# Performance work log

Hardware: AMD Instinct MI355X
Metric: run time of the kernel (lower is better)

The kernel has to match this reference:

```python
import jax, jax.numpy as jnp
import numpy as np

HEADS = 8
DIM_HEAD = 32
SCALE = DIM_HEAD ** -0.5


def setup_inputs() -> dict:
    key = jax.random.key(0)
    k1, k2, k3 = jax.random.split(key, 3)
    B, H, W, C = 16, 64, 64, 256
    hidden = HEADS * DIM_HEAD  # 256
    x = jax.random.normal(k1, (B, H, W, C), dtype=jnp.float32)
    # 1x1 convs with no bias == dense matmuls over channel dim (glorot-ish scale)
    w_qkv = jax.random.normal(k2, (C, 3 * hidden), dtype=jnp.float32) * (1.0 / np.sqrt(C))
    w_out = jax.random.normal(k3, (hidden, C), dtype=jnp.float32) * (1.0 / np.sqrt(hidden))
    return {"x": x, "w_qkv": w_qkv, "w_out": w_out}


def reference(x, w_qkv, w_out):
    B, H, W, C = x.shape
    n = H * W
    # to_qkv: 1x1 conv, no bias
    qkv = jnp.einsum('bhwc,cf->bhwf', x, w_qkv)  # [B,H,W,3*hidden]
    q, k, v = jnp.split(qkv, 3, axis=-1)

    def to_heads(t):
        # 'b x y (h c) -> b h c (x y)'
        t = t.reshape(B, n, HEADS, DIM_HEAD)
        return jnp.transpose(t, (0, 2, 3, 1))  # [B, heads, dim_head, n]

    q, k, v = to_heads(q), to_heads(k), to_heads(v)
    q = jax.nn.softmax(q, axis=-2) * SCALE      # softmax over feature dim d
    k = jax.nn.softmax(k, axis=-1)              # softmax over spatial dim n
    context = jnp.einsum('bhdn,bhen->bhde', k, v)   # [B, heads, d, e]
    out = jnp.einsum('bhde,bhdn->bhen', context, q)  # [B, heads, e, n]
    # 'b h c (x y) -> b x y (h c)'
    out = jnp.transpose(out, (0, 3, 1, 2)).reshape(B, H, W, HEADS * DIM_HEAD)
    # to_out: 1x1 conv, no bias
    return jnp.einsum('bhwf,fc->bhwc', out, w_out)
```

## Files before the change

kernel.cpp:

```cpp
#include <hip/hip_runtime.h>

using short8 = __attribute__((ext_vector_type(8))) short;
using f32x4  = __attribute__((ext_vector_type(4))) float;

#define SCALE_Q 0.17677669529663687f
#define NCHUNK 16

__device__ __forceinline__ unsigned short f2bf(float f) {
  unsigned u = __float_as_uint(f);
  return (unsigned short)((u + 0x7FFFu + ((u >> 16) & 1u)) >> 16);
}
__device__ __forceinline__ float bf2f(unsigned h) { return __uint_as_float(h << 16); }

__device__ __forceinline__ void bf8_to_f(uint4 r, float* o) {
  o[0] = bf2f(r.x & 0xffffu); o[1] = bf2f(r.x >> 16);
  o[2] = bf2f(r.y & 0xffffu); o[3] = bf2f(r.y >> 16);
  o[4] = bf2f(r.z & 0xffffu); o[5] = bf2f(r.z >> 16);
  o[6] = bf2f(r.w & 0xffffu); o[7] = bf2f(r.w >> 16);
}

__device__ __forceinline__ void gl_lds16(const unsigned short* g, unsigned short* l) {
  __builtin_amdgcn_global_load_lds(
      (const __attribute__((address_space(1))) void*)g,
      (__attribute__((address_space(3))) void*)l, 16, 0, 0);
}

__global__ __launch_bounds__(256) void prep_kernel(
    const float* __restrict__ x, const float* __restrict__ wqkv, const float* __restrict__ wout,
    unsigned short* __restrict__ xb, unsigned short* __restrict__ wqkvT,
    unsigned short* __restrict__ woutT) {
  const int blk = blockIdx.x;
  if (blk < 16384) {
    const size_t i = ((size_t)blk * 256 + threadIdx.x) * 4;
    const float4 v = *(const float4*)(x + i);
    *(ushort4*)(xb + i) = make_ushort4(f2bf(v.x), f2bf(v.y), f2bf(v.z), f2bf(v.w));
  } else if (blk < 16384 + 768) {
    const int n = blk - 16384, k = threadIdx.x;
    wqkvT[n * 256 + k] = f2bf(wqkv[(size_t)k * 768 + n]);
  } else {
    const int c = blk - 16384 - 768, f = threadIdx.x;
    woutT[c * 256 + f] = f2bf(wout[(size_t)f * 256 + c]);
  }
}

template <typename OutT, bool QSOFT, bool SWZ>
__global__ __launch_bounds__(256) void gemm_bt(
    const unsigned short* __restrict__ A, const unsigned short* __restrict__ BT,
    OutT* __restrict__ D, unsigned short* __restrict__ QS,
    int nbn, int K, int N,
    size_t strideA, size_t strideB, size_t strideD) {
  __shared__ unsigned short As[128 * 64];
  __shared__ unsigned short Bs[128 * 64];
  int lin = blockIdx.x;
  if (SWZ) {
    const int cpx = gridDim.x >> 3;
    lin = (lin & 7) * cpx + (lin >> 3);
  }
  const int bn = lin % nbn, bm = lin / nbn, bz = blockIdx.z;
  const int tid = threadIdx.x, lane = tid & 63, wid = tid >> 6;
  const int wr = wid >> 1, wc = wid & 1;
  const int fr = lane & 15, hi = lane >> 4;
  f32x4 acc[4][4] = {};
  const unsigned short* Ab = A + (size_t)bz * strideA + (size_t)bm * 128 * K;
  const unsigned short* Bb = BT + (size_t)bz * strideB + (size_t)bn * 128 * K;

  const int srow = wid * 32 + (lane >> 3);
  const int scol = (lane & 7) * 8;
  const unsigned short* Ap = Ab + (size_t)srow * K + scol;
  const unsigned short* Bp = Bb + (size_t)srow * K + scol;
  unsigned short* Asw = As + (wid * 4) * 512 + 0;
  unsigned short* Bsw = Bs + (wid * 4) * 512 + 0;

  for (int kt = 0; kt < K; kt += 64) {
#pragma unroll
    for (int i = 0; i < 4; ++i) {
      gl_lds16(Ap + (size_t)i * 8 * K + kt, Asw + i * 512);
      gl_lds16(Bp + (size_t)i * 8 * K + kt, Bsw + i * 512);
    }
    __syncthreads();
#pragma unroll
    for (int kk = 0; kk < 2; ++kk) {
      short8 af[4], bfv[4];
#pragma unroll
      for (int i = 0; i < 4; ++i) {
        af[i]  = *(const short8*)&As[(wr * 64 + i * 16 + fr) * 64 + kk * 32 + hi * 8];
        bfv[i] = *(const short8*)&Bs[(wc * 64 + i * 16 + fr) * 64 + kk * 32 + hi * 8];
      }
#pragma unroll
      for (int mi = 0; mi < 4; ++mi)
#pragma unroll
        for (int nj = 0; nj < 4; ++nj)
          acc[mi][nj] = __builtin_amdgcn_mfma_f32_16x16x32_bf16(af[mi], bfv[nj], acc[mi][nj], 0, 0, 0);
    }
    __syncthreads();
  }

  const size_t r0 = (size_t)bm * 128 + wr * 64;
  if (QSOFT && bn < 2) {
    const int c0 = bn * 128 + wc * 64;
#pragma unroll
    for (int mi = 0; mi < 4; ++mi)
#pragma unroll
      for (int p = 0; p < 2; ++p)
#pragma unroll
        for (int r = 0; r < 4; ++r) {
          const float v0 = acc[mi][2 * p][r], v1 = acc[mi][2 * p + 1][r];
          float mx = fmaxf(v0, v1);
#pragma unroll
          for (int xm = 1; xm < 16; xm <<= 1) mx = fmaxf(mx, __shfl_xor(mx, xm, 64));
          const float e0 = __expf(v0 - mx), e1 = __expf(v1 - mx);
          float s = e0 + e1;
#pragma unroll
          for (int xm = 1; xm < 16; xm <<= 1) s += __shfl_xor(s, xm, 64);
          const float inv = SCALE_Q / s;
          const size_t row = r0 + mi * 16 + hi * 4 + r;
          QS[row * 256 + c0 + p * 32 + fr]      = f2bf(e0 * inv);
          QS[row * 256 + c0 + p * 32 + 16 + fr] = f2bf(e1 * inv);
        }
    return;
  }
  const int colbase = (QSOFT ? (bn - 2) : bn) * 128 + wc * 64;
  OutT* Dz = D + (size_t)bz * strideD;
#pragma unroll
  for (int mi = 0; mi < 4; ++mi)
#pragma unroll
    for (int nj = 0; nj < 4; ++nj) {
      const int col = colbase + nj * 16 + fr;
#pragma unroll
      for (int r = 0; r < 4; ++r) {
        const size_t row = r0 + mi * 16 + hi * 4 + r;
        const float v = acc[mi][nj][r];
        if constexpr (sizeof(OutT) == 2) Dz[row * N + col] = (OutT)f2bf(v);
        else                             Dz[row * N + col] = v;
      }
    }
}

__global__ __launch_bounds__(256) void ctx_part_kernel(const unsigned short* __restrict__ kv,
                                                       float* __restrict__ part,
                                                       float* __restrict__ spart) {
  const int blk = blockIdx.x;
  const int bh = blk >> 4, chunk = blk & 15;
  const int b = bh >> 3, h = bh & 7;
  const int tid = threadIdx.x, d = tid & 31, g = tid >> 5;
  const unsigned short* kbase =
      kv + (size_t)b * 4096 * 512 + h * 32 + (size_t)chunk * 256 * 512;
  const unsigned short* vbase = kbase + 256;

  __shared__ float ek[64][36], vv[64][36];
  float a0 = 0.f, a1 = 0.f, a2 = 0.f, a3 = 0.f, ssum = 0.f;
  const int e0 = g * 4;
  const int sn = tid >> 2, sc = (tid & 3) * 8;
  const unsigned short* kp0 = kbase + (size_t)sn * 512 + sc;
  const unsigned short* vp0 = vbase + (size_t)sn * 512 + sc;
  uint4 kr = *(const uint4*)kp0;
  uint4 vr = *(const uint4*)vp0;
  for (int n0 = 0; n0 < 256; n0 += 64) {
    float kf[8], vf[8];
    bf8_to_f(kr, kf); bf8_to_f(vr, vf);
    uint4 krn = kr, vrn = vr;
    if (n0 + 64 < 256) {
      krn = *(const uint4*)(kp0 + (size_t)(n0 + 64) * 512);
      vrn = *(const uint4*)(vp0 + (size_t)(n0 + 64) * 512);
    }
#pragma unroll
    for (int j = 0; j < 8; ++j) { ek[sn][sc + j] = __expf(kf[j]); vv[sn][sc + j] = vf[j]; }
    __syncthreads();
#pragma unroll 8
    for (int i = 0; i < 64; ++i) {
      const float kd = ek[i][d];
      const float4 v4 = *(const float4*)&vv[i][e0];
      ssum += kd;
      a0 += kd * v4.x; a1 += kd * v4.y; a2 += kd * v4.z; a3 += kd * v4.w;
    }
    __syncthreads();
    kr = krn; vr = vrn;
  }
  float* pp = part + ((size_t)chunk * 128 + bh) * 1024 + d * 32 + e0;
  pp[0] = a0; pp[1] = a1; pp[2] = a2; pp[3] = a3;
  if (g == 0) spart[((size_t)chunk * 128 + bh) * 32 + d] = ssum;
}

__global__ __launch_bounds__(256) void ctx_combine_kernel(const float* __restrict__ part,
                                                          const float* __restrict__ spart,
                                                          float* __restrict__ ctx) {
  const int bh = blockIdx.x, tid = threadIdx.x;
  __shared__ float sinv[32];
  if (tid < 32) {
    float s = 0.f;
#pragma unroll
    for (int c = 0; c < NCHUNK; ++c) s += spart[((size_t)c * 128 + bh) * 32 + tid];
    sinv[tid] = 1.0f / s;
  }
  __syncthreads();
  float4 acc = make_float4(0.f, 0.f, 0.f, 0.f);
#pragma unroll
  for (int c = 0; c < NCHUNK; ++c) {
    const float4 p = *(const float4*)(part + ((size_t)c * 128 + bh) * 1024 + tid * 4);
    acc.x += p.x; acc.y += p.y; acc.z += p.z; acc.w += p.w;
  }
  const float si = sinv[tid >> 3];
  float4* cp = (float4*)(ctx + (size_t)bh * 1024 + tid * 4);
  *cp = make_float4(acc.x * si, acc.y * si, acc.z * si, acc.w * si);
}

__global__ __launch_bounds__(256) void w2_kernel(const float* __restrict__ ctx,
                                                 const unsigned short* __restrict__ woutT,
                                                 unsigned short* __restrict__ W2T) {
  const int b = blockIdx.x >> 4, cg = blockIdx.x & 15;
  const int tid = threadIdx.x;
  __shared__ float cs[8 * 32 * 32];
  {
    const float4* src = (const float4*)(ctx + (size_t)b * 8192);
    float4* dst = (float4*)cs;
#pragma unroll
    for (int i = 0; i < 8; ++i) dst[tid + i * 256] = src[tid + i * 256];
  }
  __syncthreads();
  const int c = cg * 16 + (tid >> 4), chunk = tid & 15;
  const int h = chunk >> 1, d0 = (chunk & 1) * 16;
  float wf[32];
  {
    const uint4* wp = (const uint4*)(woutT + (size_t)c * 256 + h * 32);
    bf8_to_f(wp[0], wf + 0); bf8_to_f(wp[1], wf + 8);
    bf8_to_f(wp[2], wf + 16); bf8_to_f(wp[3], wf + 24);
  }
  unsigned short o[16];
#pragma unroll
  for (int dd = 0; dd < 16; ++dd) {
    const float* cp = cs + h * 1024 + (d0 + dd) * 32;
    float acc = 0.f;
#pragma unroll
    for (int e = 0; e < 32; ++e) acc += cp[e] * wf[e];
    o[dd] = f2bf(acc);
  }
  uint4* op = (uint4*)(W2T + ((size_t)b * 256 + c) * 256 + chunk * 16);
  op[0] = make_uint4((unsigned)o[0] | ((unsigned)o[1] << 16), (unsigned)o[2] | ((unsigned)o[3] << 16),
                     (unsigned)o[4] | ((unsigned)o[5] << 16), (unsigned)o[6] | ((unsigned)o[7] << 16));
  op[1] = make_uint4((unsigned)o[8] | ((unsigned)o[9] << 16), (unsigned)o[10] | ((unsigned)o[11] << 16),
                     (unsigned)o[12] | ((unsigned)o[13] << 16), (unsigned)o[14] | ((unsigned)o[15] << 16));
}

extern "C" void kernel_launch(void* const* d_in, const int* in_sizes, int n_in,
                              void* d_out, int out_size, void* d_ws, size_t ws_size,
                              hipStream_t stream) {
  const float* x     = (const float*)d_in[0];
  const float* wqkv  = (const float*)d_in[1];
  const float* wout  = (const float*)d_in[2];
  float* out = (float*)d_out;

  char* ws = (char*)d_ws;
  unsigned short* xb    = (unsigned short*)(ws);
  unsigned short* wqkvT = (unsigned short*)(ws + 33554432);
  unsigned short* woutT = (unsigned short*)(ws + 33947648);
  unsigned short* kv    = (unsigned short*)(ws + 34078720);
  float*          ctx   = (float*)        (ws + 101187584);
  unsigned short* qs    = (unsigned short*)(ws + 101711872);
  float*          part  = (float*)(ws);
  float*          spart = (float*)(ws + 8388608);
  unsigned short* W2T   = (unsigned short*)(ws + 12582912);

  prep_kernel<<<16384 + 768 + 256, 256, 0, stream>>>(x, wqkv, wout, xb, wqkvT, woutT);
  gemm_bt<unsigned short, true, true><<<3072, 256, 0, stream>>>(
      xb, wqkvT, kv, qs, 6, 256, 512, 0, 0, 0);
  ctx_part_kernel<<<2048, 256, 0, stream>>>(kv, part, spart);
  ctx_combine_kernel<<<128, 256, 0, stream>>>(part, spart, ctx);
  w2_kernel<<<256, 256, 0, stream>>>(ctx, woutT, W2T);
  gemm_bt<float, false, false><<<dim3(64, 1, 16), 256, 0, stream>>>(
      qs, W2T, out, nullptr, 2, 256, 256, (size_t)4096 * 256, (size_t)256 * 256, (size_t)4096 * 256);
}
```

Before: 175.0 us.

## Keep GEMM B strip in registers and stream full-K A tiles through swizzled LDS

Both GEMMs are replaced by a kernel in which each block loads a 64-column strip of the weight matrix into registers once. It then loops over several 128-row A tiles, loading the full K=256 into LDS with an XOR swizzle to avoid bank conflicts. This cuts repeated B traffic and the per-k-tile syncs, and maps groups of tiles to XCDs for L2 locality. In exchange it uses many more registers (128 VGPRs for B), a 64 KB LDS tile and no load/compute overlap within a block, so occupancy may drop.

```diff
diff --git a/kernel.cpp b/kernel.cpp
--- a/kernel.cpp
+++ b/kernel.cpp
@@ -43,97 +43,97 @@
   }
 }
 
-template <typename OutT, bool QSOFT, bool SWZ>
-__global__ __launch_bounds__(256) void gemm_bt(
+template <typename OutT, bool QKV>
+__global__ __launch_bounds__(256, 2) void gemm_bregs(
     const unsigned short* __restrict__ A, const unsigned short* __restrict__ BT,
     OutT* __restrict__ D, unsigned short* __restrict__ QS,
-    int nbn, int K, int N,
+    int NSTRIP, int TPB,
     size_t strideA, size_t strideB, size_t strideD) {
-  __shared__ unsigned short As[128 * 64];
-  __shared__ unsigned short Bs[128 * 64];
-  int lin = blockIdx.x;
-  if (SWZ) {
-    const int cpx = gridDim.x >> 3;
-    lin = (lin & 7) * cpx + (lin >> 3);
-  }
-  const int bn = lin % nbn, bm = lin / nbn, bz = blockIdx.z;
+  __shared__ unsigned short As[128 * 256];
+  const int xcd = blockIdx.x & 7, idx = blockIdx.x >> 3;
+  const int strip = idx % NSTRIP;
+  const int mg = xcd + (idx / NSTRIP) * 8;
+  const int z = blockIdx.z;
   const int tid = threadIdx.x, lane = tid & 63, wid = tid >> 6;
-  const int wr = wid >> 1, wc = wid & 1;
   const int fr = lane & 15, hi = lane >> 4;
-  f32x4 acc[4][4] = {};
-  const unsigned short* Ab = A + (size_t)bz * strideA + (size_t)bm * 128 * K;
-  const unsigned short* Bb = BT + (size_t)bz * strideB + (size_t)bn * 128 * K;
-
-  const int srow = wid * 32 + (lane >> 3);
-  const int scol = (lane & 7) * 8;
-  const unsigned short* Ap = Ab + (size_t)srow * K + scol;
-  const unsigned short* Bp = Bb + (size_t)srow * K + scol;
-  unsigned short* Asw = As + (wid * 4) * 512 + 0;
-  unsigned short* Bsw = Bs + (wid * 4) * 512 + 0;
-
-  for (int kt = 0; kt < K; kt += 64) {
-#pragma unroll
-    for (int i = 0; i < 4; ++i) {
-      gl_lds16(Ap + (size_t)i * 8 * K + kt, Asw + i * 512);
-      gl_lds16(Bp + (size_t)i * 8 * K + kt, Bsw + i * 512);
-    }
-    __syncthreads();
-#pragma unroll
-    for (int kk = 0; kk < 2; ++kk) {
-      short8 af[4], bfv[4];
-#pragma unroll
-      for (int i = 0; i < 4; ++i) {
-        af[i]  = *(const short8*)&As[(wr * 64 + i * 16 + fr) * 64 + kk * 32 + hi * 8];
-        bfv[i] = *(const short8*)&Bs[(wc * 64 + i * 16 + fr) * 64 + kk * 32 + hi * 8];
+
+  const unsigned short* Bb = BT + (size_t)z * strideB + (size_t)strip * 64 * 256;
+  short8 breg[4][8];
+#pragma unroll
+  for (int nj = 0; nj < 4; ++nj)
+#pragma unroll
+    for (int kk = 0; kk < 8; ++kk)
+      breg[nj][kk] = *(const short8*)(Bb + (size_t)(nj * 16 + fr) * 256 + kk * 32 + hi * 8);
+
+  const int srow = tid >> 5;
+  const int schunk = (tid & 31) ^ srow;
+  const size_t sgoff = (size_t)srow * 256 + schunk * 8;
+  unsigned short* lds_w = As + wid * 512;
+
+  for (int t = 0; t < TPB; ++t) {
+    const size_t row0 = (size_t)(mg * TPB + t) * 128;
+    const unsigned short* Ag = A + (size_t)z * strideA + row0 * 256 + sgoff;
+#pragma unroll
+    for (int r = 0; r < 16; ++r) gl_lds16(Ag + r * 2048, lds_w + r * 2048);
+    __syncthreads();
+
+    f32x4 acc[2][4] = {};
+#pragma unroll
+    for (int kk = 0; kk < 8; ++kk) {
+      short8 af[2];
+#pragma unroll
+      for (int mi = 0; mi < 2; ++mi) {
+        const int row = wid * 32 + mi * 16 + fr;
+        const int ch = (kk * 4 + hi) ^ (fr & 7);
+        af[mi] = *(const short8*)&As[row * 256 + ch * 8];
       }
 #pragma unroll
-      for (int mi = 0; mi < 4; ++mi)
+      for (int mi = 0; mi < 2; ++mi)
 #pragma unroll
         for (int nj = 0; nj < 4; ++nj)
-          acc[mi][nj] = __builtin_amdgcn_mfma_f32_16x16x32_bf16(af[mi], bfv[nj], acc[mi][nj], 0, 0, 0);
-    }
-    __syncthreads();
-  }
-
-  const size_t r0 = (size_t)bm * 128 + wr * 64;
-  if (QSOFT && bn < 2) {
-    const int c0 = bn * 128 + wc * 64;
-#pragma unroll
-    for (int mi = 0; mi < 4; ++mi)
-#pragma unroll
-      for (int p = 0; p < 2; ++p)
-#pragma unroll
-        for (int r = 0; r < 4; ++r) {
-          const float v0 = acc[mi][2 * p][r], v1 = acc[mi][2 * p + 1][r];
-          float mx = fmaxf(v0, v1);
-#pragma unroll
-          for (int xm = 1; xm < 16; xm <<= 1) mx = fmaxf(mx, __shfl_xor(mx, xm, 64));
-          const float e0 = __expf(v0 - mx), e1 = __expf(v1 - mx);
-          float s = e0 + e1;
-#pragma unroll
-          for (int xm = 1; xm < 16; xm <<= 1) s += __shfl_xor(s, xm, 64);
-          const float inv = SCALE_Q / s;
-          const size_t row = r0 + mi * 16 + hi * 4 + r;
-          QS[row * 256 + c0 + p * 32 + fr]      = f2bf(e0 * inv);
-          QS[row * 256 + c0 + p * 32 + 16 + fr] = f2bf(e1 * inv);
+          acc[mi][nj] = __builtin_amdgcn_mfma_f32_16x16x32_bf16(af[mi], breg[nj][kk], acc[mi][nj], 0, 0, 0);
+    }
+
+    if (QKV && strip < 4) {
+#pragma unroll
+      for (int mi = 0; mi < 2; ++mi)
+#pragma unroll
+        for (int p = 0; p < 2; ++p)
+#pragma unroll
+          for (int r = 0; r < 4; ++r) {
+            const float v0 = acc[mi][2 * p][r], v1 = acc[mi][2 * p + 1][r];
+            float mx = fmaxf(v0, v1);
+#pragma unroll
+            for (int xm = 1; xm < 16; xm <<= 1) mx = fmaxf(mx, __shfl_xor(mx, xm, 64));
+            const float e0 = __expf(v0 - mx), e1 = __expf(v1 - mx);
+            float s = e0 + e1;
+#pragma unroll
+            for (int xm = 1; xm < 16; xm <<= 1) s += __shfl_xor(s, xm, 64);
+            const float inv = SCALE_Q / s;
+            const size_t row = row0 + wid * 32 + mi * 16 + hi * 4 + r;
+            QS[row * 256 + strip * 64 + p * 32 + fr]      = f2bf(e0 * inv);
+            QS[row * 256 + strip * 64 + p * 32 + 16 + fr] = f2bf(e1 * inv);
+          }
+    } else {
+      const int c0 = QKV ? (strip * 64 - 256) : (strip * 64);
+      const int ncols = QKV ? 512 : 256;
+      OutT* Dz = D + (size_t)z * strideD;
+#pragma unroll
+      for (int mi = 0; mi < 2; ++mi)
+#pragma unroll
+        for (int nj = 0; nj < 4; ++nj) {
+          const int col = c0 + nj * 16 + fr;
+#pragma unroll
+          for (int r = 0; r < 4; ++r) {
+            const size_t row = row0 + wid * 32 + mi * 16 + hi * 4 + r;
+            const float v = acc[mi][nj][r];
+            if constexpr (sizeof(OutT) == 2) Dz[row * ncols + col] = (OutT)f2bf(v);
+            else                             Dz[row * ncols + col] = v;
+          }
         }
-    return;
-  }
-  const int colbase = (QSOFT ? (bn - 2) : bn) * 128 + wc * 64;
-  OutT* Dz = D + (size_t)bz * strideD;
-#pragma unroll
-  for (int mi = 0; mi < 4; ++mi)
-#pragma unroll
-    for (int nj = 0; nj < 4; ++nj) {
-      const int col = colbase + nj * 16 + fr;
-#pragma unroll
-      for (int r = 0; r < 4; ++r) {
-        const size_t row = r0 + mi * 16 + hi * 4 + r;
-        const float v = acc[mi][nj][r];
-        if constexpr (sizeof(OutT) == 2) Dz[row * N + col] = (OutT)f2bf(v);
-        else                             Dz[row * N + col] = v;
-      }
-    }
+    }
+    __syncthreads();
+  }
 }
 
 __global__ __launch_bounds__(256) void ctx_part_kernel(const unsigned short* __restrict__ kv,
@@ -261,11 +261,12 @@
   unsigned short* W2T   = (unsigned short*)(ws + 12582912);
 
   prep_kernel<<<16384 + 768 + 256, 256, 0, stream>>>(x, wqkv, wout, xb, wqkvT, woutT);
-  gemm_bt<unsigned short, true, true><<<3072, 256, 0, stream>>>(
-      xb, wqkvT, kv, qs, 6, 256, 512, 0, 0, 0);
+  gemm_bregs<unsigned short, true><<<1536, 256, 0, stream>>>(
+      xb, wqkvT, kv, qs, 12, 4, 0, 0, 0);
   ctx_part_kernel<<<2048, 256, 0, stream>>>(kv, part, spart);
   ctx_combine_kernel<<<128, 256, 0, stream>>>(part, spart, ctx);
   w2_kernel<<<256, 256, 0, stream>>>(ctx, woutT, W2T);
-  gemm_bt<float, false, false><<<dim3(64, 1, 16), 256, 0, stream>>>(
-      qs, W2T, out, nullptr, 2, 256, 256, (size_t)4096 * 256, (size_t)256 * 256, (size_t)4096 * 256);
-}
+  gemm_bregs<float, false><<<dim3(32, 1, 16), 256, 0, stream>>>(
+      qs, W2T, out, nullptr, 4, 4,
+      (size_t)4096 * 256, (size_t)256 * 256, (size_t)4096 * 256);
+}
```

Measured after the change: 177.4 us. About the same (+1.4%).

## Stage GEMM tiles through registers into padded LDS with a 32-wide K step

Applied to the files above, without the earlier changes.

The bf16 GEMM kernel no longer uses direct global-to-LDS loads. Each thread now loads 16-byte vectors into registers and writes them into LDS tiles padded to 40 columns, with the K step cut from 64 to 32. The padding is meant to remove LDS bank conflicts on the short8 fragment reads. The cost is twice as many barriers per K loop, extra register traffic and less in-flight memory per iteration. The output GEMM now takes its block coordinates from a 2D grid, and the row stride is derived from the template instead of a runtime argument.

```diff
diff --git a/kernel.cpp b/kernel.cpp
--- a/kernel.cpp
+++ b/kernel.cpp
@@ -17,12 +17,6 @@
   o[2] = bf2f(r.y & 0xffffu); o[3] = bf2f(r.y >> 16);
   o[4] = bf2f(r.z & 0xffffu); o[5] = bf2f(r.z >> 16);
   o[6] = bf2f(r.w & 0xffffu); o[7] = bf2f(r.w >> 16);
-}
-
-__device__ __forceinline__ void gl_lds16(const unsigned short* g, unsigned short* l) {
-  __builtin_amdgcn_global_load_lds(
-      (const __attribute__((address_space(1))) void*)g,
-      (__attribute__((address_space(3))) void*)l, 16, 0, 0);
 }
 
 __global__ __launch_bounds__(256) void prep_kernel(
@@ -47,51 +41,44 @@
 __global__ __launch_bounds__(256) void gemm_bt(
     const unsigned short* __restrict__ A, const unsigned short* __restrict__ BT,
     OutT* __restrict__ D, unsigned short* __restrict__ QS,
-    int nbn, int K, int N,
+    int nbn, int K,
     size_t strideA, size_t strideB, size_t strideD) {
-  __shared__ unsigned short As[128 * 64];
-  __shared__ unsigned short Bs[128 * 64];
-  int lin = blockIdx.x;
+  __shared__ unsigned short As[128][40];
+  __shared__ unsigned short Bs[128][40];
+  int bn, bm;
   if (SWZ) {
     const int cpx = gridDim.x >> 3;
-    lin = (lin & 7) * cpx + (lin >> 3);
-  }
-  const int bn = lin % nbn, bm = lin / nbn, bz = blockIdx.z;
+    const int lin = ((int)blockIdx.x & 7) * cpx + ((int)blockIdx.x >> 3);
+    bn = lin % nbn; bm = lin / nbn;
+  } else {
+    bn = blockIdx.x; bm = blockIdx.y;
+  }
+  const int bz = blockIdx.z;
   const int tid = threadIdx.x, lane = tid & 63, wid = tid >> 6;
   const int wr = wid >> 1, wc = wid & 1;
-  const int fr = lane & 15, hi = lane >> 4;
+  const int fr = lane & 15, hi = lane >> 4, fk = hi * 8;
   f32x4 acc[4][4] = {};
-  const unsigned short* Ab = A + (size_t)bz * strideA + (size_t)bm * 128 * K;
-  const unsigned short* Bb = BT + (size_t)bz * strideB + (size_t)bn * 128 * K;
-
-  const int srow = wid * 32 + (lane >> 3);
-  const int scol = (lane & 7) * 8;
-  const unsigned short* Ap = Ab + (size_t)srow * K + scol;
-  const unsigned short* Bp = Bb + (size_t)srow * K + scol;
-  unsigned short* Asw = As + (wid * 4) * 512 + 0;
-  unsigned short* Bsw = Bs + (wid * 4) * 512 + 0;
-
-  for (int kt = 0; kt < K; kt += 64) {
+  const size_t abase = (size_t)bz * strideA + (size_t)bm * 128 * K;
+  const size_t bbase = (size_t)bz * strideB + (size_t)bn * 128 * K;
+
+  for (int kt = 0; kt < K; kt += 32) {
+    for (int c = tid; c < 512; c += 256) {
+      const int row = c >> 2, kc = (c & 3) * 8;
+      *(uint4*)&As[row][kc] = *(const uint4*)(A + abase + (size_t)row * K + kt + kc);
+      *(uint4*)&Bs[row][kc] = *(const uint4*)(BT + bbase + (size_t)row * K + kt + kc);
+    }
+    __syncthreads();
+    short8 af[4], bfv[4];
 #pragma unroll
     for (int i = 0; i < 4; ++i) {
-      gl_lds16(Ap + (size_t)i * 8 * K + kt, Asw + i * 512);
-      gl_lds16(Bp + (size_t)i * 8 * K + kt, Bsw + i * 512);
-    }
-    __syncthreads();
-#pragma unroll
-    for (int kk = 0; kk < 2; ++kk) {
-      short8 af[4], bfv[4];
-#pragma unroll
-      for (int i = 0; i < 4; ++i) {
-        af[i]  = *(const short8*)&As[(wr * 64 + i * 16 + fr) * 64 + kk * 32 + hi * 8];
-        bfv[i] = *(const short8*)&Bs[(wc * 64 + i * 16 + fr) * 64 + kk * 32 + hi * 8];
-      }
-#pragma unroll
-      for (int mi = 0; mi < 4; ++mi)
-#pragma unroll
-        for (int nj = 0; nj < 4; ++nj)
-          acc[mi][nj] = __builtin_amdgcn_mfma_f32_16x16x32_bf16(af[mi], bfv[nj], acc[mi][nj], 0, 0, 0);
-    }
+      af[i]  = *(const short8*)&As[wr * 64 + i * 16 + fr][fk];
+      bfv[i] = *(const short8*)&Bs[wc * 64 + i * 16 + fr][fk];
+    }
+#pragma unroll
+    for (int mi = 0; mi < 4; ++mi)
+#pragma unroll
+      for (int nj = 0; nj < 4; ++nj)
+        acc[mi][nj] = __builtin_amdgcn_mfma_f32_16x16x32_bf16(af[mi], bfv[nj], acc[mi][nj], 0, 0, 0);
     __syncthreads();
   }
 
@@ -120,6 +107,7 @@
     return;
   }
   const int colbase = (QSOFT ? (bn - 2) : bn) * 128 + wc * 64;
+  const int ncols = QSOFT ? 512 : 256;
   OutT* Dz = D + (size_t)bz * strideD;
 #pragma unroll
   for (int mi = 0; mi < 4; ++mi)
@@ -130,8 +118,8 @@
       for (int r = 0; r < 4; ++r) {
         const size_t row = r0 + mi * 16 + hi * 4 + r;
         const float v = acc[mi][nj][r];
-        if constexpr (sizeof(OutT) == 2) Dz[row * N + col] = (OutT)f2bf(v);
-        else                             Dz[row * N + col] = v;
+        if constexpr (sizeof(OutT) == 2) Dz[row * ncols + col] = (OutT)f2bf(v);
+        else                             Dz[row * ncols + col] = v;
       }
     }
 }
@@ -262,10 +250,11 @@
 
   prep_kernel<<<16384 + 768 + 256, 256, 0, stream>>>(x, wqkv, wout, xb, wqkvT, woutT);
   gemm_bt<unsigned short, true, true><<<3072, 256, 0, stream>>>(
-      xb, wqkvT, kv, qs, 6, 256, 512, 0, 0, 0);
+      xb, wqkvT, kv, qs, 6, 256, 0, 0, 0);
   ctx_part_kernel<<<2048, 256, 0, stream>>>(kv, part, spart);
   ctx_combine_kernel<<<128, 256, 0, stream>>>(part, spart, ctx);
   w2_kernel<<<256, 256, 0, stream>>>(ctx, woutT, W2T);
-  gemm_bt<float, false, false><<<dim3(64, 1, 16), 256, 0, stream>>>(
-      qs, W2T, out, nullptr, 2, 256, 256, (size_t)4096 * 256, (size_t)256 * 256, (size_t)4096 * 256);
-}
+  gemm_bt<float, false, false><<<dim3(2, 32, 16), 256, 0, stream>>>(
+      qs, W2T, out, nullptr, 2, 256,
+      (size_t)4096 * 256, (size_t)256 * 256, (size_t)4096 * 256);
+}
```

Measured after the change: 166.7 us. -4.8%, faster.
